# Kernel optimization log

Measured on AMD Instinct MI355X. Metric: run time of the kernel, lower is better.

## Reference

```python
import jax, jax.numpy as jnp
import numpy as np

N, E, IN_DIM, HID, LAT, G = 100000, 1600000, 64, 128, 64, 1000
BN_EPS = 1e-5
LN_EPS = 1e-5


def _bn(x, g, b, m, v):
    # BatchNorm1d in eval mode: running stats
    return (x - m) * jax.lax.rsqrt(v + BN_EPS) * g + b


def setup_inputs() -> dict:
    key = jax.random.key(0)
    ks = iter(jax.random.split(key, 64))
    d = {}
    d["x"] = jax.random.normal(next(ks), (N, IN_DIM), jnp.float32)
    d["edge_index"] = jax.random.randint(next(ks), (2, E), 0, N, jnp.int32)
    d["batch"] = jnp.sort(jax.random.randint(next(ks), (N,), 0, G, jnp.int32))

    def lin(k, i, o):
        k1, k2 = jax.random.split(k)
        s = 1.0 / np.sqrt(i)
        return (jax.random.uniform(k1, (i, o), jnp.float32, -s, s),
                jax.random.uniform(k2, (o,), jnp.float32, -s, s))

    def bn_params(k, dim):
        g = 1.0 + 0.1 * jax.random.normal(k, (dim,), jnp.float32)
        return g, jnp.zeros(dim), jnp.zeros(dim), jnp.ones(dim)

    # input BN
    d["in_g"], d["in_b"], d["in_m"], d["in_v"] = bn_params(next(ks), IN_DIM)
    # conv layer 0 (in_dim -> hid)
    d["eps0"] = jnp.zeros(())
    d["c0_w1"], d["c0_b1"] = lin(next(ks), IN_DIM, HID)
    d["c0_g"], d["c0_bb"], d["c0_m"], d["c0_v"] = bn_params(next(ks), HID)
    d["c0_w2"], d["c0_b2"] = lin(next(ks), HID, HID)
    d["bn0_g"], d["bn0_b"], d["bn0_m"], d["bn0_v"] = bn_params(next(ks), HID)
    # conv layers 1..2 stacked (hid -> hid)
    def stack(fn):
        a = [fn(next(ks)) for _ in range(2)]
        return tuple(jnp.stack([t[i] for t in a]) for i in range(len(a[0])))
    d["epsR"] = jnp.zeros((2,))
    d["cR_w1"], d["cR_b1"] = stack(lambda k: lin(k, HID, HID))
    d["cR_g"], d["cR_bb"], d["cR_m"], d["cR_v"] = stack(lambda k: bn_params(k, HID))
    d["cR_w2"], d["cR_b2"] = stack(lambda k: lin(k, HID, HID))
    d["bnR_g"], d["bnR_b"], d["bnR_m"], d["bnR_v"] = stack(lambda k: bn_params(k, HID))
    # head
    d["fc1_w"], d["fc1_b"] = lin(next(ks), HID, HID)
    d["ln_g"] = jnp.ones(HID); d["ln_b"] = jnp.zeros(HID)
    d["fc2_w"], d["fc2_b"] = lin(next(ks), HID, LAT)
    return d


def _gin_layer(x, src, dst, eps, w1, b1, g, bb, m, v, w2, b2, og, ob, om, ov):
    # GINConv with sum aggregation: (1+eps)*x + scatter_sum(x[src] -> dst)
    agg = jax.ops.segment_sum(x[src], dst, num_segments=N)
    h = (1.0 + eps) * x + agg
    # GatedResidualMLP: Linear -> BN -> GELU -> (dropout off) -> Linear
    h = _bn(h @ w1 + b1, g, bb, m, v)
    h = jax.nn.gelu(h, approximate=False)
    h = h @ w2 + b2
    # outer BN -> GELU
    return jax.nn.gelu(_bn(h, og, ob, om, ov), approximate=False)


def reference(x, edge_index, batch, in_g, in_b, in_m, in_v,
              eps0, c0_w1, c0_b1, c0_g, c0_bb, c0_m, c0_v, c0_w2, c0_b2,
              bn0_g, bn0_b, bn0_m, bn0_v,
              epsR, cR_w1, cR_b1, cR_g, cR_bb, cR_m, cR_v, cR_w2, cR_b2,
              bnR_g, bnR_b, bnR_m, bnR_v,
              fc1_w, fc1_b, ln_g, ln_b, fc2_w, fc2_b):
    src, dst = edge_index[0], edge_index[1]
    h = _bn(x, in_g, in_b, in_m, in_v)
    h = _gin_layer(h, src, dst, eps0, c0_w1, c0_b1, c0_g, c0_bb, c0_m, c0_v,
                   c0_w2, c0_b2, bn0_g, bn0_b, bn0_m, bn0_v)
    for l in range(2):
        h = _gin_layer(h, src, dst, epsR[l], cR_w1[l], cR_b1[l], cR_g[l],
                       cR_bb[l], cR_m[l], cR_v[l], cR_w2[l], cR_b2[l],
                       bnR_g[l], bnR_b[l], bnR_m[l], bnR_v[l])
    # global mean pool over graphs
    sums = jax.ops.segment_sum(h, batch, num_segments=G)
    cnt = jax.ops.segment_sum(jnp.ones((N,), h.dtype), batch, num_segments=G)
    pooled = sums / jnp.maximum(cnt, 1.0)[:, None]
    # head: fc1 -> LayerNorm -> GELU -> residual -> fc2
    o = pooled @ fc1_w + fc1_b
    mu = jnp.mean(o, -1, keepdims=True)
    var = jnp.var(o, -1, keepdims=True)
    o = (o - mu) * jax.lax.rsqrt(var + LN_EPS) * ln_g + ln_b
    o = jax.nn.gelu(o, approximate=False) + pooled
    return o @ fc2_w + fc2_b
```

## Files before the change

kernel.cpp:

```cpp
#include <hip/hip_runtime.h>

#define BN_EPS 1e-5f
#define LN_EPS 1e-5f

typedef unsigned int uint;
typedef unsigned short ushort;
typedef __bf16 bf16_t;
typedef bf16_t bf16x8 __attribute__((ext_vector_type(8)));
typedef float f32x4 __attribute__((ext_vector_type(4)));

__device__ __forceinline__ float gelu_exact(float x){
    return 0.5f * x * (1.0f + erff(x * 0.7071067811865475f));
}
__device__ __forceinline__ float gelu_fast(float x){
    float z = x*(0.79788456f + 0.03567740814f*(x*x));
    z = fminf(fmaxf(z, -15.f), 15.f);
    float t = __builtin_amdgcn_exp2f(2.885390082f*z);
    return x*t*__builtin_amdgcn_rcpf(t + 1.0f);
}
__device__ __forceinline__ ushort f2bf(float f){
    union { float f; uint u; } x; x.f = f;
    uint r = (x.u + 0x7FFF + ((x.u >> 16) & 1)) >> 16;
    return (ushort)r;
}
__device__ __forceinline__ float bf2f(ushort u){
    union { uint u; float f; } x; x.u = ((uint)u) << 16;
    return x.f;
}

__global__ void zero_i32(int* __restrict__ p, int n){
    int i = blockIdx.x*blockDim.x + threadIdx.x;
    if (i < n) p[i] = 0;
}
__global__ void zero_f32(float* __restrict__ p, int n){
    int i = blockIdx.x*blockDim.x + threadIdx.x;
    if (i < n) p[i] = 0.0f;
}

__global__ void bn_input(const float* __restrict__ x,
                         const float* __restrict__ g, const float* __restrict__ b,
                         const float* __restrict__ m, const float* __restrict__ v,
                         ushort* __restrict__ out, int n4){
    int i = blockIdx.x*blockDim.x + threadIdx.x;
    if (i >= n4) return;
    int c0 = (i & 15) * 4;
    float4 xv = ((const float4*)x)[i];
    ushort o[4];
    #pragma unroll
    for (int j = 0; j < 4; j++){
        int c = c0 + j;
        float s  = g[c] * rsqrtf(v[c] + BN_EPS);
        float sh = b[c] - m[c]*s;
        o[j] = f2bf((&xv.x)[j]*s + sh);
    }
    uint2 pk = make_uint2((uint)o[0] | ((uint)o[1]<<16), (uint)o[2] | ((uint)o[3]<<16));
    ((uint2*)out)[i] = pk;
}

__global__ void pack_w(const float* __restrict__ w, ushort* __restrict__ out, int K){
    int t = blockIdx.x*blockDim.x + threadIdx.x;
    int total = (K/32)*8*64;
    if (t >= total) return;
    int lane = t & 63;
    int rem = t >> 6;
    int nf = rem & 7;
    int kk = rem >> 3;
    int kg = lane >> 4;
    int col = nf*16 + (lane & 15);
    uint r[4];
    #pragma unroll
    for (int p = 0; p < 4; p++){
        int k0 = kk*32 + kg*8 + p*2;
        ushort lo = f2bf(w[(size_t)k0*128 + col]);
        ushort hi = f2bf(w[(size_t)(k0+1)*128 + col]);
        r[p] = (uint)lo | ((uint)hi << 16);
    }
    *(uint4*)(out + (size_t)t*8) = make_uint4(r[0], r[1], r[2], r[3]);
}


__global__ __launch_bounds__(256) void bucket_count(const int* __restrict__ dst,
        int* __restrict__ bcnt, int E, int NB){
    __shared__ int h[1024];
    int tid = threadIdx.x;
    for (int i = tid; i < 1024; i += 256) h[i] = 0;
    __syncthreads();
    for (long i = (long)blockIdx.x*blockDim.x + tid; i < E; i += (long)gridDim.x*blockDim.x)
        atomicAdd(&h[dst[i] >> 8], 1);
    __syncthreads();
    for (int i = tid; i < NB; i += 256)
        if (h[i]) atomicAdd(&bcnt[i], h[i]);
}

__global__ __launch_bounds__(1024) void bucket_scan(const int* __restrict__ bcnt,
        int* __restrict__ boff, int* __restrict__ bcur, int NB, int E){
    __shared__ int s[1024];
    int tid = threadIdx.x;
    int v = (tid < NB) ? bcnt[tid] : 0;
    s[tid] = v; __syncthreads();
    for (int off = 1; off < 1024; off <<= 1){
        int t = s[tid];
        if (tid >= off) t += s[tid-off];
        __syncthreads(); s[tid] = t; __syncthreads();
    }
    if (tid < NB){ int ex = s[tid] - v; boff[tid] = ex; bcur[tid] = ex; }
    if (tid == 0) boff[NB] = E;
}

#define PCH 16384
__global__ __launch_bounds__(512) void partition_kernel(const int* __restrict__ src,
        const int* __restrict__ dst, int* __restrict__ bcur,
        uint* __restrict__ pairs, int E, int NB){
    __shared__ ushort rnk[PCH];
    __shared__ int cnt[1024];
    __shared__ int base[1024];
    int tid = threadIdx.x;
    long chunk0 = (long)blockIdx.x * PCH;
    for (int i = tid; i < 1024; i += 512) cnt[i] = 0;
    __syncthreads();
    for (int k = 0; k < PCH/512; k++){
        int el = k*512 + tid;
        long i = chunk0 + el;
        if (i < E){
            int b = dst[i] >> 8;
            rnk[el] = (ushort)atomicAdd(&cnt[b], 1);
        }
    }
    __syncthreads();
    for (int b = tid; b < NB; b += 512)
        if (cnt[b] > 0) base[b] = atomicAdd(&bcur[b], cnt[b]);
    __syncthreads();
    for (int k = 0; k < PCH/512; k++){
        int el = k*512 + tid;
        long i = chunk0 + el;
        if (i < E){
            int d = dst[i];
            int b = d >> 8;
            int pos = base[b] + (int)rnk[el];
            pairs[pos] = ((uint)(d & 255) << 24) | (uint)src[i];
        }
    }
}

#define BCAP 12288
__global__ __launch_bounds__(256) void bucket_build(const uint* __restrict__ pairs,
        const int* __restrict__ boff, int* __restrict__ rowptr,
        int* __restrict__ csrc, int N, int E, int NB){
    __shared__ int deg[256];
    __shared__ int scn[256];
    __shared__ int cur[256];
    __shared__ uint outl[BCAP];
    int b = blockIdx.x, tid = threadIdx.x;
    int e0 = boff[b], e1 = boff[b+1];
    int M = e1 - e0;
    deg[tid] = 0;
    __syncthreads();
    for (int e = tid; e < M; e += 256){
        uint p = pairs[e0 + e];
        atomicAdd(&deg[p >> 24], 1);
    }
    __syncthreads();
    int v = deg[tid];
    scn[tid] = v; __syncthreads();
    for (int off = 1; off < 256; off <<= 1){
        int t = scn[tid];
        if (tid >= off) t += scn[tid-off];
        __syncthreads(); scn[tid] = t; __syncthreads();
    }
    int excl = scn[tid] - v;
    int node = b*256 + tid;
    if (node < N) rowptr[node] = e0 + excl;
    if (b == NB-1 && tid == 0) rowptr[N] = E;
    cur[tid] = excl;
    __syncthreads();
    if (M <= BCAP){
        for (int e = tid; e < M; e += 256){
            uint p = pairs[e0 + e];
            int lp = atomicAdd(&cur[p >> 24], 1);
            outl[lp] = p & 0x00FFFFFFu;
        }
        __syncthreads();
        for (int e = tid; e < M; e += 256)
            csrc[e0 + e] = (int)(outl[e]);
    } else {
        for (int e = tid; e < M; e += 256){
            uint p = pairs[e0 + e];
            int lp = atomicAdd(&cur[p >> 24], 1);
            csrc[e0 + lp] = (int)(p & 0x00FFFFFFu);
        }
    }
}

__global__ __launch_bounds__(256) void agg_d64(const ushort* __restrict__ hin,
        const int* __restrict__ rowptr, const int* __restrict__ csrc,
        const float* __restrict__ epsp, int epsidx,
        ushort* __restrict__ hout, int n){
    int w = __builtin_amdgcn_readfirstlane(blockIdx.x*4 + (threadIdx.x >> 6));
    if (w >= n) return;
    int lane = threadIdx.x & 63;
    float eps1 = 1.0f + epsp[epsidx];
    int beg = __builtin_amdgcn_readfirstlane(rowptr[w]);
    int end = __builtin_amdgcn_readfirstlane(rowptr[w+1]);
    float acc = 0.0f;
    int j = beg;
    for (; j + 16 <= end; j += 16){
        ushort t[16];
        #pragma unroll
        for (int u = 0; u < 16; u++){
            int su = __builtin_amdgcn_readfirstlane(csrc[j+u]);
            t[u] = hin[((size_t)su << 6) + lane];
        }
        #pragma unroll
        for (int u = 0; u < 16; u++) acc += bf2f(t[u]);
    }
    if (j < end){
        int last = end - 1;
        ushort t[16];
        #pragma unroll
        for (int u = 0; u < 16; u++){
            int jj = j + u; jj = jj < last ? jj : last;
            int su = __builtin_amdgcn_readfirstlane(csrc[jj]);
            t[u] = hin[((size_t)su << 6) + lane];
        }
        #pragma unroll
        for (int u = 0; u < 16; u++){
            ushort tv = (j + u) < end ? t[u] : (ushort)0;
            acc += bf2f(tv);
        }
    }
    float self = bf2f(hin[((size_t)w << 6) + lane]);
    hout[((size_t)w << 6) + lane] = f2bf(eps1*self + acc);
}

__global__ __launch_bounds__(256) void agg_d128(const ushort* __restrict__ hin,
        const int* __restrict__ rowptr, const int* __restrict__ csrc,
        const float* __restrict__ epsp, int epsidx,
        ushort* __restrict__ hout, int n){
    int w = __builtin_amdgcn_readfirstlane(blockIdx.x*4 + (threadIdx.x >> 6));
    if (w >= n) return;
    int lane = threadIdx.x & 63;
    float eps1 = 1.0f + epsp[epsidx];
    int beg = __builtin_amdgcn_readfirstlane(rowptr[w]);
    int end = __builtin_amdgcn_readfirstlane(rowptr[w+1]);
    const uint* h2 = (const uint*)hin;
    float ax = 0.f, ay = 0.f;
    int j = beg;
    for (; j + 16 <= end; j += 16){
        uint t[16];
        #pragma unroll
        for (int u = 0; u < 16; u++){
            int su = __builtin_amdgcn_readfirstlane(csrc[j+u]);
            t[u] = h2[((size_t)su << 6) + lane];
        }
        #pragma unroll
        for (int u = 0; u < 16; u++){
            ax += bf2f((ushort)(t[u] & 0xFFFF));
            ay += bf2f((ushort)(t[u] >> 16));
        }
    }
    if (j < end){
        int last = end - 1;
        uint t[16];
        #pragma unroll
        for (int u = 0; u < 16; u++){
            int jj = j + u; jj = jj < last ? jj : last;
            int su = __builtin_amdgcn_readfirstlane(csrc[jj]);
            t[u] = h2[((size_t)su << 6) + lane];
        }
        #pragma unroll
        for (int u = 0; u < 16; u++){
            uint tv = (j + u) < end ? t[u] : 0u;
            ax += bf2f((ushort)(tv & 0xFFFF));
            ay += bf2f((ushort)(tv >> 16));
        }
    }
    uint c = h2[((size_t)w << 6) + lane];
    float ox = eps1*bf2f((ushort)(c & 0xFFFF)) + ax;
    float oy = eps1*bf2f((ushort)(c >> 16)) + ay;
    ((uint*)hout)[((size_t)w << 6) + lane] = (uint)f2bf(ox) | ((uint)f2bf(oy) << 16);
}

template<int DIN>
__global__ __launch_bounds__(256) void mlp_mfma(
        const ushort* __restrict__ hin,
        const ushort* __restrict__ w1p, const float* __restrict__ b1,
        const float* __restrict__ g1, const float* __restrict__ bb1,
        const float* __restrict__ m1, const float* __restrict__ v1,
        const ushort* __restrict__ w2p, const float* __restrict__ b2,
        const float* __restrict__ g2, const float* __restrict__ bb2,
        const float* __restrict__ m2, const float* __restrict__ v2,
        ushort* __restrict__ hout, int n)
{
    constexpr int K1 = DIN/32;
    __shared__ ushort lds[128*128];
    __shared__ float mulA[128], addA[128], mulB[128], addB[128];
    int tid = threadIdx.x;
    int lane = tid & 63;
    int wv = tid >> 6;
    int row0 = blockIdx.x * 128;

    if (tid < 128){
        float s1 = g1[tid]*rsqrtf(v1[tid]+BN_EPS);
        mulA[tid] = s1; addA[tid] = (b1[tid]-m1[tid])*s1 + bb1[tid];
        float s2 = g2[tid]*rsqrtf(v2[tid]+BN_EPS);
        mulB[tid] = s2; addB[tid] = (b2[tid]-m2[tid])*s2 + bb2[tid];
    }

    bf16x8 wpre[8];
    #pragma unroll
    for (int nf = 0; nf < 8; nf++)
        wpre[nf] = *(const bf16x8*)(w1p + ((size_t)(nf*64 + lane))*8);

    constexpr int CPR = DIN/8;
    for (int idx = tid; idx < 128*CPR; idx += 256){
        int r = idx / CPR, c = idx - r*CPR;
        uint4 val = make_uint4(0,0,0,0);
        if (row0 + r < n) val = *(const uint4*)(hin + (size_t)(row0+r)*DIN + c*8);
        int byte = (r*DIN + c*8)*2 ^ ((r & 7) << 4);
        *(uint4*)((char*)lds + byte) = val;
    }
    __syncthreads();

    int r16 = lane & 15;
    int kg = lane >> 4;
    int arow = wv*32 + r16;

    f32x4 acc[2][8];
    #pragma unroll
    for (int m = 0; m < 2; m++)
        #pragma unroll
        for (int nf = 0; nf < 8; nf++) acc[m][nf] = (f32x4){0.f,0.f,0.f,0.f};
    #pragma unroll
    for (int kk = 0; kk < K1; kk++){
        int ab0 = (arow*DIN + kk*32 + kg*8)*2 ^ ((arow & 7) << 4);
        bf16x8 a0 = *(const bf16x8*)((const char*)lds + ab0);
        bf16x8 a1 = *(const bf16x8*)((const char*)lds + ab0 + DIN*32);
        #pragma unroll
        for (int nf = 0; nf < 8; nf++){
            bf16x8 w = (kk == 0) ? wpre[nf]
                     : *(const bf16x8*)(w1p + ((size_t)((kk*8 + nf)*64 + lane))*8);
            acc[0][nf] = __builtin_amdgcn_mfma_f32_16x16x32_bf16(a0, w, acc[0][nf], 0, 0, 0);
            acc[1][nf] = __builtin_amdgcn_mfma_f32_16x16x32_bf16(a1, w, acc[1][nf], 0, 0, 0);
        }
    }

    if constexpr (DIN == 64) __syncthreads();

    bf16x8 wpre2[8];
    #pragma unroll
    for (int nf = 0; nf < 8; nf++)
        wpre2[nf] = *(const bf16x8*)(w2p + ((size_t)(nf*64 + lane))*8);

    #pragma unroll
    for (int m = 0; m < 2; m++){
        #pragma unroll
        for (int nf = 0; nf < 8; nf++){
            int col = nf*16 + r16;
            float mu = mulA[col], ad = addA[col];
            #pragma unroll
            for (int r = 0; r < 4; r++){
                int row = wv*32 + m*16 + kg*4 + r;
                float xg = gelu_fast(acc[m][nf][r]*mu + ad);
                int byte = (row*128 + col)*2 ^ ((row & 7) << 4);
                *(ushort*)((char*)lds + byte) = f2bf(xg);
            }
        }
    }

    f32x4 acc2[2][8];
    #pragma unroll
    for (int m = 0; m < 2; m++)
        #pragma unroll
        for (int nf = 0; nf < 8; nf++) acc2[m][nf] = (f32x4){0.f,0.f,0.f,0.f};
    #pragma unroll
    for (int kk = 0; kk < 4; kk++){
        int ab0 = (arow*128 + kk*32 + kg*8)*2 ^ ((arow & 7) << 4);
        bf16x8 a0 = *(const bf16x8*)((const char*)lds + ab0);
        bf16x8 a1 = *(const bf16x8*)((const char*)lds + ab0 + 128*32);
        #pragma unroll
        for (int nf = 0; nf < 8; nf++){
            bf16x8 w = (kk == 0) ? wpre2[nf]
                     : *(const bf16x8*)(w2p + ((size_t)((kk*8 + nf)*64 + lane))*8);
            acc2[0][nf] = __builtin_amdgcn_mfma_f32_16x16x32_bf16(a0, w, acc2[0][nf], 0, 0, 0);
            acc2[1][nf] = __builtin_amdgcn_mfma_f32_16x16x32_bf16(a1, w, acc2[1][nf], 0, 0, 0);
        }
    }

    #pragma unroll
    for (int m = 0; m < 2; m++){
        #pragma unroll
        for (int nf = 0; nf < 8; nf++){
            int col = nf*16 + r16;
            float mu = mulB[col], ad = addB[col];
            #pragma unroll
            for (int r = 0; r < 4; r++){
                int row = wv*32 + m*16 + kg*4 + r;
                float xg = gelu_fast(acc2[m][nf][r]*mu + ad);
                int byte = (row*128 + col)*2 ^ ((row & 7) << 4);
                *(ushort*)((char*)lds + byte) = f2bf(xg);
            }
        }
    }
    __syncthreads();

    for (int idx = tid; idx < 128*16; idx += 256){
        int r = idx >> 4, c = idx & 15;
        if (row0 + r < n){
            int byte = (r*128 + c*8)*2 ^ ((r & 7) << 4);
            uint4 v = *(const uint4*)((const char*)lds + byte);
            *(uint4*)(hout + (size_t)(row0+r)*128 + c*8) = v;
        }
    }
}

__global__ __launch_bounds__(128) void pool_kernel(const ushort* __restrict__ h,
        const int* __restrict__ batch, float* __restrict__ pool,
        float* __restrict__ cnt, int n){
    int c = threadIdx.x;
    int n0 = blockIdx.x * 32;
    float run = 0.f;
    float runc = 0.f;
    int curg = -1;
    for (int t = 0; t < 32; ++t){
        int node = n0 + t;
        if (node >= n) break;
        int gph = batch[node];
        if (gph != curg){
            if (curg >= 0){
                atomicAdd(&pool[curg*128 + c], run);
                if (c == 0) atomicAdd(&cnt[curg], runc);
            }
            curg = gph; run = 0.f; runc = 0.f;
        }
        run += bf2f(h[(size_t)node*128 + c]);
        runc += 1.f;
    }
    if (curg >= 0){
        atomicAdd(&pool[curg*128 + c], run);
        if (c == 0) atomicAdd(&cnt[curg], runc);
    }
}

__global__ __launch_bounds__(128) void head_kernel(const float* __restrict__ pool,
        const float* __restrict__ cnt,
        const float* __restrict__ fc1w, const float* __restrict__ fc1b,
        const float* __restrict__ lng, const float* __restrict__ lnb,
        const float* __restrict__ fc2w, const float* __restrict__ fc2b,
        float* __restrict__ out, int G){
    __shared__ float p[128];
    __shared__ float q[128];
    __shared__ float red[128];
    int g = blockIdx.x, c = threadIdx.x;
    float inv = 1.0f / fmaxf(cnt[g], 1.0f);
    float pv = pool[g*128 + c] * inv;
    p[c] = pv;
    __syncthreads();
    float o = fc1b[c];
    for (int k = 0; k < 128; k++) o = fmaf(p[k], fc1w[k*128 + c], o);
    red[c] = o; __syncthreads();
    for (int s = 64; s > 0; s >>= 1){ if (c < s) red[c] += red[c+s]; __syncthreads(); }
    float mu = red[0] * (1.0f/128.0f);
    __syncthreads();
    float d = o - mu;
    red[c] = d*d; __syncthreads();
    for (int s = 64; s > 0; s >>= 1){ if (c < s) red[c] += red[c+s]; __syncthreads(); }
    float var = red[0] * (1.0f/128.0f);
    __syncthreads();
    float xn = d * rsqrtf(var + LN_EPS) * lng[c] + lnb[c];
    float qv = gelu_exact(xn) + pv;
    q[c] = qv;
    __syncthreads();
    if (c < 64){
        float a = fc2b[c];
        for (int k = 0; k < 128; k++) a = fmaf(q[k], fc2w[k*64 + c], a);
        out[g*64 + c] = a;
    }
}

extern "C" void kernel_launch(void* const* d_in, const int* in_sizes, int n_in,
                              void* d_out, int out_size, void* d_ws, size_t ws_size,
                              hipStream_t stream){
    const float* x     = (const float*)d_in[0];
    const int*   ei    = (const int*)d_in[1];
    const int*   batch = (const int*)d_in[2];
    const float* in_g  = (const float*)d_in[3];
    const float* in_b  = (const float*)d_in[4];
    const float* in_m  = (const float*)d_in[5];
    const float* in_v  = (const float*)d_in[6];
    const float* eps0  = (const float*)d_in[7];
    const float* c0_w1 = (const float*)d_in[8];
    const float* c0_b1 = (const float*)d_in[9];
    const float* c0_g  = (const float*)d_in[10];
    const float* c0_bb = (const float*)d_in[11];
    const float* c0_m  = (const float*)d_in[12];
    const float* c0_v  = (const float*)d_in[13];
    const float* c0_w2 = (const float*)d_in[14];
    const float* c0_b2 = (const float*)d_in[15];
    const float* bn0_g = (const float*)d_in[16];
    const float* bn0_b = (const float*)d_in[17];
    const float* bn0_m = (const float*)d_in[18];
    const float* bn0_v = (const float*)d_in[19];
    const float* epsR  = (const float*)d_in[20];
    const float* cR_w1 = (const float*)d_in[21];
    const float* cR_b1 = (const float*)d_in[22];
    const float* cR_g  = (const float*)d_in[23];
    const float* cR_bb = (const float*)d_in[24];
    const float* cR_m  = (const float*)d_in[25];
    const float* cR_v  = (const float*)d_in[26];
    const float* cR_w2 = (const float*)d_in[27];
    const float* cR_b2 = (const float*)d_in[28];
    const float* bnR_g = (const float*)d_in[29];
    const float* bnR_b = (const float*)d_in[30];
    const float* bnR_m = (const float*)d_in[31];
    const float* bnR_v = (const float*)d_in[32];
    const float* fc1_w = (const float*)d_in[33];
    const float* fc1_b = (const float*)d_in[34];
    const float* ln_g  = (const float*)d_in[35];
    const float* ln_b  = (const float*)d_in[36];
    const float* fc2_w = (const float*)d_in[37];
    const float* fc2_b = (const float*)d_in[38];

    const int N = in_sizes[0] / 64;
    const int E = in_sizes[1] / 2;
    const int G = out_size / 64;
    const int NB = (N + 255) >> 8;
    const int* srcp = ei;
    const int* dstp = ei + E;

    char* ws = (char*)d_ws;
    size_t off = 0;
    auto alloc = [&](size_t bytes)->char*{
        char* p = ws + off;
        off = (off + bytes + 255) & ~(size_t)255;
        return p;
    };
    ushort* bufA   = (ushort*)alloc((size_t)N*128*2);
    ushort* bufB   = (ushort*)alloc((size_t)N*128*2);
    int*    rowptr = (int*)   alloc((size_t)(N+1)*4);
    int*    csrc   = (int*)   alloc((size_t)E*4);
    uint*   pairs  = (uint*)  alloc((size_t)E*4);
    int*    bcnt   = (int*)   alloc((size_t)1025*4);
    int*    boff   = (int*)   alloc((size_t)1025*4);
    int*    bcur   = (int*)   alloc((size_t)1024*4);
    float*  pool   = (float*) alloc((size_t)G*128*4);
    float*  cnt    = (float*) alloc((size_t)G*4);
    ushort* pw0_1  = (ushort*)alloc((size_t)64*128*2);
    ushort* pw0_2  = (ushort*)alloc((size_t)128*128*2);
    ushort* pwR_1  = (ushort*)alloc((size_t)2*128*128*2);
    ushort* pwR_2  = (ushort*)alloc((size_t)2*128*128*2);
    (void)ws_size; (void)n_in;

    pack_w<<<(1024 + 255)/256, 256, 0, stream>>>(c0_w1, pw0_1, 64);
    pack_w<<<(2048 + 255)/256, 256, 0, stream>>>(c0_w2, pw0_2, 128);
    for (int l = 0; l < 2; l++){
        pack_w<<<(2048 + 255)/256, 256, 0, stream>>>(cR_w1 + (size_t)l*128*128, pwR_1 + (size_t)l*128*128, 128);
        pack_w<<<(2048 + 255)/256, 256, 0, stream>>>(cR_w2 + (size_t)l*128*128, pwR_2 + (size_t)l*128*128, 128);
    }

    zero_i32<<<(NB + 255)/256, 256, 0, stream>>>(bcnt, NB);
    bucket_count<<<1024, 256, 0, stream>>>(dstp, bcnt, E, NB);
    bucket_scan<<<1, 1024, 0, stream>>>(bcnt, boff, bcur, NB, E);
    partition_kernel<<<(E + PCH-1)/PCH, 512, 0, stream>>>(srcp, dstp, bcur, pairs, E, NB);
    bucket_build<<<NB, 256, 0, stream>>>(pairs, boff, rowptr, csrc, N, E, NB);

    bn_input<<<(N*16 + 255)/256, 256, 0, stream>>>(x, in_g, in_b, in_m, in_v, bufA, N*16);

    const int agg_blocks = (N + 3)/4;
    const int mlp_blocks = (N + 127)/128;

    agg_d64<<<agg_blocks, 256, 0, stream>>>(bufA, rowptr, csrc, eps0, 0, bufB, N);
    mlp_mfma<64><<<mlp_blocks, 256, 0, stream>>>(bufB,
        pw0_1, c0_b1, c0_g, c0_bb, c0_m, c0_v,
        pw0_2, c0_b2, bn0_g, bn0_b, bn0_m, bn0_v, bufA, N);

    for (int l = 0; l < 2; l++){
        agg_d128<<<agg_blocks, 256, 0, stream>>>(bufA, rowptr, csrc, epsR, l, bufB, N);
        mlp_mfma<128><<<mlp_blocks, 256, 0, stream>>>(bufB,
            pwR_1 + (size_t)l*128*128, cR_b1 + l*128, cR_g + l*128, cR_bb + l*128,
            cR_m + l*128, cR_v + l*128,
            pwR_2 + (size_t)l*128*128, cR_b2 + l*128, bnR_g + l*128, bnR_b + l*128,
            bnR_m + l*128, bnR_v + l*128, bufA, N);
    }

    zero_f32<<<(G*128 + 255)/256, 256, 0, stream>>>(pool, G*128);
    zero_f32<<<(G + 255)/256, 256, 0, stream>>>(cnt, G);
    pool_kernel<<<(N + 31)/32, 128, 0, stream>>>(bufA, batch, pool, cnt, N);
    head_kernel<<<G, 128, 0, stream>>>(pool, cnt, fc1_w, fc1_b, ln_g, ln_b,
                                       fc2_w, fc2_b, (float*)d_out, G);
}
```

Measured before the change: 375.2 us.

## Store node features in column-block slices to shrink gather working set

Producers (input BN and the first MLPs) now write features in column-sliced layout, with 16-channel blocks stored contiguously per node. The aggregation kernels assign each block one channel slice, so each gather touches a 32-byte row segment and the per-slice array is small enough to stay cache-resident. Each wave gathers eight neighbors at once with lanes split across neighbors, then reduces across lanes with shuffles. The cost is eight times more aggregation passes over the CSR indices, extra shuffle reductions, and scattered 32-byte writes from the MLP epilogue.

```diff
diff --git a/kernel.cpp b/kernel.cpp
--- a/kernel.cpp
+++ b/kernel.cpp
@@ -40,9 +40,10 @@
 __global__ void bn_input(const float* __restrict__ x,
                          const float* __restrict__ g, const float* __restrict__ b,
                          const float* __restrict__ m, const float* __restrict__ v,
-                         ushort* __restrict__ out, int n4){
+                         uint* __restrict__ outs, int n4, int n){
     int i = blockIdx.x*blockDim.x + threadIdx.x;
     if (i >= n4) return;
+    int node = i >> 4;
     int c0 = (i & 15) * 4;
     float4 xv = ((const float4*)x)[i];
     ushort o[4];
@@ -54,7 +55,9 @@
         o[j] = f2bf((&xv.x)[j]*s + sh);
     }
     uint2 pk = make_uint2((uint)o[0] | ((uint)o[1]<<16), (uint)o[2] | ((uint)o[3]<<16));
-    ((uint2*)out)[i] = pk;
+    int cb = c0 >> 4;
+    size_t pos = (size_t)cb*((size_t)n*8) + (size_t)node*8 + ((c0 & 15) >> 1);
+    *(uint2*)(outs + pos) = pk;
 }
 
 __global__ void pack_w(const float* __restrict__ w, ushort* __restrict__ out, int K){
@@ -191,96 +194,126 @@
     }
 }
 
-__global__ __launch_bounds__(256) void agg_d64(const ushort* __restrict__ hin,
+
+__global__ __launch_bounds__(256) void agg_s128(
+        const uint* __restrict__ hs,
         const int* __restrict__ rowptr, const int* __restrict__ csrc,
         const float* __restrict__ epsp, int epsidx,
-        ushort* __restrict__ hout, int n){
-    int w = __builtin_amdgcn_readfirstlane(blockIdx.x*4 + (threadIdx.x >> 6));
-    if (w >= n) return;
+        uint* __restrict__ hout, int n)
+{
+    int cb = blockIdx.x & 7;
+    int ng = blockIdx.x >> 3;
     int lane = threadIdx.x & 63;
+    int wv = threadIdx.x >> 6;
+    int u = lane >> 3;
+    int c = lane & 7;
     float eps1 = 1.0f + epsp[epsidx];
-    int beg = __builtin_amdgcn_readfirstlane(rowptr[w]);
-    int end = __builtin_amdgcn_readfirstlane(rowptr[w+1]);
-    float acc = 0.0f;
-    int j = beg;
-    for (; j + 16 <= end; j += 16){
-        ushort t[16];
-        #pragma unroll
-        for (int u = 0; u < 16; u++){
-            int su = __builtin_amdgcn_readfirstlane(csrc[j+u]);
-            t[u] = hin[((size_t)su << 6) + lane];
-        }
-        #pragma unroll
-        for (int u = 0; u < 16; u++) acc += bf2f(t[u]);
-    }
-    if (j < end){
-        int last = end - 1;
-        ushort t[16];
-        #pragma unroll
-        for (int u = 0; u < 16; u++){
+    const uint* slice = hs + (size_t)cb * ((size_t)n * 8);
+    int node0 = (ng*4 + wv) * 8;
+    #pragma unroll 1
+    for (int t = 0; t < 8; t++){
+        int node = node0 + t;
+        if (node >= n) return;
+        int beg = __builtin_amdgcn_readfirstlane(rowptr[node]);
+        int end = __builtin_amdgcn_readfirstlane(rowptr[node+1]);
+        float a0 = 0.f, a1 = 0.f;
+        int j = beg;
+        for (; j + 16 <= end; j += 16){
+            int s0 = __builtin_nontemporal_load(&csrc[j + u]);
+            int s1 = __builtin_nontemporal_load(&csrc[j + 8 + u]);
+            uint t0 = slice[(size_t)s0*8 + c];
+            uint t1 = slice[(size_t)s1*8 + c];
+            a0 += bf2f((ushort)(t0 & 0xFFFF)); a1 += bf2f((ushort)(t0 >> 16));
+            a0 += bf2f((ushort)(t1 & 0xFFFF)); a1 += bf2f((ushort)(t1 >> 16));
+        }
+        for (; j + 8 <= end; j += 8){
+            int s0 = __builtin_nontemporal_load(&csrc[j + u]);
+            uint t0 = slice[(size_t)s0*8 + c];
+            a0 += bf2f((ushort)(t0 & 0xFFFF)); a1 += bf2f((ushort)(t0 >> 16));
+        }
+        if (j < end){
+            int last = end - 1;
             int jj = j + u; jj = jj < last ? jj : last;
-            int su = __builtin_amdgcn_readfirstlane(csrc[jj]);
-            t[u] = hin[((size_t)su << 6) + lane];
-        }
-        #pragma unroll
-        for (int u = 0; u < 16; u++){
-            ushort tv = (j + u) < end ? t[u] : (ushort)0;
-            acc += bf2f(tv);
-        }
-    }
-    float self = bf2f(hin[((size_t)w << 6) + lane]);
-    hout[((size_t)w << 6) + lane] = f2bf(eps1*self + acc);
-}
-
-__global__ __launch_bounds__(256) void agg_d128(const ushort* __restrict__ hin,
+            int s0 = __builtin_nontemporal_load(&csrc[jj]);
+            uint t0 = slice[(size_t)s0*8 + c];
+            if (j + u < end){
+                a0 += bf2f((ushort)(t0 & 0xFFFF)); a1 += bf2f((ushort)(t0 >> 16));
+            }
+        }
+        #pragma unroll
+        for (int m = 8; m <= 32; m <<= 1){
+            a0 += __shfl_xor(a0, m, 64);
+            a1 += __shfl_xor(a1, m, 64);
+        }
+        if (lane < 8){
+            uint sv = slice[(size_t)node*8 + lane];
+            float o0 = eps1*bf2f((ushort)(sv & 0xFFFF)) + a0;
+            float o1 = eps1*bf2f((ushort)(sv >> 16))    + a1;
+            hout[(size_t)node*64 + cb*8 + lane] = (uint)f2bf(o0) | ((uint)f2bf(o1) << 16);
+        }
+    }
+}
+
+__global__ __launch_bounds__(256) void agg_s64(
+        const uint* __restrict__ hs,
         const int* __restrict__ rowptr, const int* __restrict__ csrc,
         const float* __restrict__ epsp, int epsidx,
-        ushort* __restrict__ hout, int n){
-    int w = __builtin_amdgcn_readfirstlane(blockIdx.x*4 + (threadIdx.x >> 6));
-    if (w >= n) return;
+        uint* __restrict__ hout, int n)
+{
+    int cb = blockIdx.x & 3;
+    int ng = blockIdx.x >> 2;
     int lane = threadIdx.x & 63;
+    int wv = threadIdx.x >> 6;
+    int u = lane >> 3;
+    int c = lane & 7;
     float eps1 = 1.0f + epsp[epsidx];
-    int beg = __builtin_amdgcn_readfirstlane(rowptr[w]);
-    int end = __builtin_amdgcn_readfirstlane(rowptr[w+1]);
-    const uint* h2 = (const uint*)hin;
-    float ax = 0.f, ay = 0.f;
-    int j = beg;
-    for (; j + 16 <= end; j += 16){
-        uint t[16];
-        #pragma unroll
-        for (int u = 0; u < 16; u++){
-            int su = __builtin_amdgcn_readfirstlane(csrc[j+u]);
-            t[u] = h2[((size_t)su << 6) + lane];
-        }
-        #pragma unroll
-        for (int u = 0; u < 16; u++){
-            ax += bf2f((ushort)(t[u] & 0xFFFF));
-            ay += bf2f((ushort)(t[u] >> 16));
-        }
-    }
-    if (j < end){
-        int last = end - 1;
-        uint t[16];
-        #pragma unroll
-        for (int u = 0; u < 16; u++){
+    const uint* slice = hs + (size_t)cb * ((size_t)n * 8);
+    int node0 = (ng*4 + wv) * 8;
+    #pragma unroll 1
+    for (int t = 0; t < 8; t++){
+        int node = node0 + t;
+        if (node >= n) return;
+        int beg = __builtin_amdgcn_readfirstlane(rowptr[node]);
+        int end = __builtin_amdgcn_readfirstlane(rowptr[node+1]);
+        float a0 = 0.f, a1 = 0.f;
+        int j = beg;
+        for (; j + 16 <= end; j += 16){
+            int s0 = __builtin_nontemporal_load(&csrc[j + u]);
+            int s1 = __builtin_nontemporal_load(&csrc[j + 8 + u]);
+            uint t0 = slice[(size_t)s0*8 + c];
+            uint t1 = slice[(size_t)s1*8 + c];
+            a0 += bf2f((ushort)(t0 & 0xFFFF)); a1 += bf2f((ushort)(t0 >> 16));
+            a0 += bf2f((ushort)(t1 & 0xFFFF)); a1 += bf2f((ushort)(t1 >> 16));
+        }
+        for (; j + 8 <= end; j += 8){
+            int s0 = __builtin_nontemporal_load(&csrc[j + u]);
+            uint t0 = slice[(size_t)s0*8 + c];
+            a0 += bf2f((ushort)(t0 & 0xFFFF)); a1 += bf2f((ushort)(t0 >> 16));
+        }
+        if (j < end){
+            int last = end - 1;
             int jj = j + u; jj = jj < last ? jj : last;
-            int su = __builtin_amdgcn_readfirstlane(csrc[jj]);
-            t[u] = h2[((size_t)su << 6) + lane];
-        }
-        #pragma unroll
-        for (int u = 0; u < 16; u++){
-            uint tv = (j + u) < end ? t[u] : 0u;
-            ax += bf2f((ushort)(tv & 0xFFFF));
-            ay += bf2f((ushort)(tv >> 16));
-        }
-    }
-    uint c = h2[((size_t)w << 6) + lane];
-    float ox = eps1*bf2f((ushort)(c & 0xFFFF)) + ax;
-    float oy = eps1*bf2f((ushort)(c >> 16)) + ay;
-    ((uint*)hout)[((size_t)w << 6) + lane] = (uint)f2bf(ox) | ((uint)f2bf(oy) << 16);
-}
-
-template<int DIN>
+            int s0 = __builtin_nontemporal_load(&csrc[jj]);
+            uint t0 = slice[(size_t)s0*8 + c];
+            if (j + u < end){
+                a0 += bf2f((ushort)(t0 & 0xFFFF)); a1 += bf2f((ushort)(t0 >> 16));
+            }
+        }
+        #pragma unroll
+        for (int m = 8; m <= 32; m <<= 1){
+            a0 += __shfl_xor(a0, m, 64);
+            a1 += __shfl_xor(a1, m, 64);
+        }
+        if (lane < 8){
+            uint sv = slice[(size_t)node*8 + lane];
+            float o0 = eps1*bf2f((ushort)(sv & 0xFFFF)) + a0;
+            float o1 = eps1*bf2f((ushort)(sv >> 16))    + a1;
+            hout[(size_t)node*32 + cb*8 + lane] = (uint)f2bf(o0) | ((uint)f2bf(o1) << 16);
+        }
+    }
+}
+
+template<int DIN, bool SPLIT_OUT>
 __global__ __launch_bounds__(256) void mlp_mfma(
         const ushort* __restrict__ hin,
         const ushort* __restrict__ w1p, const float* __restrict__ b1,
@@ -404,11 +437,17 @@
     __syncthreads();
 
     for (int idx = tid; idx < 128*16; idx += 256){
-        int r = idx >> 4, c = idx & 15;
+        int r = idx >> 4, cseg = idx & 15;
         if (row0 + r < n){
-            int byte = (r*128 + c*8)*2 ^ ((r & 7) << 4);
+            int byte = (r*128 + cseg*8)*2 ^ ((r & 7) << 4);
             uint4 v = *(const uint4*)((const char*)lds + byte);
-            *(uint4*)(hout + (size_t)(row0+r)*128 + c*8) = v;
+            if constexpr (SPLIT_OUT){
+                int cb = cseg >> 1;
+                size_t pos = (size_t)cb*((size_t)n*8) + (size_t)(row0+r)*8 + (cseg & 1)*4;
+                *(uint4*)((uint*)hout + pos) = v;
+            } else {
+                *(uint4*)(hout + (size_t)(row0+r)*128 + cseg*8) = v;
+            }
         }
     }
 }
@@ -563,24 +602,32 @@
     partition_kernel<<<(E + PCH-1)/PCH, 512, 0, stream>>>(srcp, dstp, bcur, pairs, E, NB);
     bucket_build<<<NB, 256, 0, stream>>>(pairs, boff, rowptr, csrc, N, E, NB);
 
-    bn_input<<<(N*16 + 255)/256, 256, 0, stream>>>(x, in_g, in_b, in_m, in_v, bufA, N*16);
-
-    const int agg_blocks = (N + 3)/4;
+    bn_input<<<(N*16 + 255)/256, 256, 0, stream>>>(x, in_g, in_b, in_m, in_v,
+                                                   (uint*)bufA, N*16, N);
+
+    const int aggs64_blocks  = ((N + 31)/32)*4;
+    const int aggs128_blocks = ((N + 31)/32)*8;
     const int mlp_blocks = (N + 127)/128;
 
-    agg_d64<<<agg_blocks, 256, 0, stream>>>(bufA, rowptr, csrc, eps0, 0, bufB, N);
-    mlp_mfma<64><<<mlp_blocks, 256, 0, stream>>>(bufB,
+    agg_s64<<<aggs64_blocks, 256, 0, stream>>>((const uint*)bufA, rowptr, csrc,
+                                               eps0, 0, (uint*)bufB, N);
+    mlp_mfma<64,true><<<mlp_blocks, 256, 0, stream>>>(bufB,
         pw0_1, c0_b1, c0_g, c0_bb, c0_m, c0_v,
         pw0_2, c0_b2, bn0_g, bn0_b, bn0_m, bn0_v, bufA, N);
 
-    for (int l = 0; l < 2; l++){
-        agg_d128<<<agg_blocks, 256, 0, stream>>>(bufA, rowptr, csrc, epsR, l, bufB, N);
-        mlp_mfma<128><<<mlp_blocks, 256, 0, stream>>>(bufB,
-            pwR_1 + (size_t)l*128*128, cR_b1 + l*128, cR_g + l*128, cR_bb + l*128,
-            cR_m + l*128, cR_v + l*128,
-            pwR_2 + (size_t)l*128*128, cR_b2 + l*128, bnR_g + l*128, bnR_b + l*128,
-            bnR_m + l*128, bnR_v + l*128, bufA, N);
-    }
+    agg_s128<<<aggs128_blocks, 256, 0, stream>>>((const uint*)bufA, rowptr, csrc,
+                                                 epsR, 0, (uint*)bufB, N);
+    mlp_mfma<128,true><<<mlp_blocks, 256, 0, stream>>>(bufB,
+        pwR_1, cR_b1, cR_g, cR_bb, cR_m, cR_v,
+        pwR_2, cR_b2, bnR_g, bnR_b, bnR_m, bnR_v, bufA, N);
+
+    agg_s128<<<aggs128_blocks, 256, 0, stream>>>((const uint*)bufA, rowptr, csrc,
+                                                 epsR, 1, (uint*)bufB, N);
+    mlp_mfma<128,false><<<mlp_blocks, 256, 0, stream>>>(bufB,
+        pwR_1 + (size_t)128*128, cR_b1 + 128, cR_g + 128, cR_bb + 128,
+        cR_m + 128, cR_v + 128,
+        pwR_2 + (size_t)128*128, cR_b2 + 128, bnR_g + 128, bnR_b + 128,
+        bnR_m + 128, bnR_v + 128, bufA, N);
 
     zero_f32<<<(G*128 + 255)/256, 256, 0, stream>>>(pool, G*128);
     zero_f32<<<(G + 255)/256, 256, 0, stream>>>(cnt, G);
```

Measured after the change: 926.6 us. 147% more time.
